# Kernel tuning notes

Measured on AMD Instinct MI355X. Metric: run time of the kernel, lower is better.

The kernel has to match this reference:

```python
import jax, jax.numpy as jnp
import numpy as np

B = 32                 # decode batch (sequences)
NBLK = 128             # blocks per sequence
BLOCK = 16             # tokens per block
H, D = 16, 128         # heads, head_dim
HID = H * D            # 2048
FFN = 8192
VOCAB = 32000
MAXPOS = 8192
KV_LEN = NBLK * BLOCK  # 2048 max context
NUM_BLOCKS = B * NBLK  # 4096
ROPE_THETA = 10000.0


def _rope_cos_sin(pos):
    # pos: [...] int -> cos, sin: [..., D//2]
    inv_freq = 1.0 / (ROPE_THETA ** (jnp.arange(0, D, 2, dtype=jnp.float32) / D))
    ang = pos.astype(jnp.float32)[..., None] * inv_freq
    return jnp.cos(ang), jnp.sin(ang)


def _apply_rope(x, cos, sin):
    # x: [..., D]; cos/sin broadcastable to [..., D//2]; half-split (Llama) rotation
    x1, x2 = jnp.split(x, 2, axis=-1)
    return jnp.concatenate([x1 * cos - x2 * sin, x1 * sin + x2 * cos], axis=-1)


def setup_inputs() -> dict:
    key = jax.random.key(0)
    ks = jax.random.split(key, 12)
    inp = {
        "input_ids": jax.random.randint(ks[0], (B,), 0, VOCAB),
        "positions": jax.random.randint(ks[1], (B,), 0, KV_LEN),
        "kv_cache": jax.random.normal(ks[2], (NUM_BLOCKS, 2, BLOCK, H, D), jnp.float32),
        "block_tables": jnp.arange(NUM_BLOCKS, dtype=jnp.int32).reshape(B, NBLK),
        "context_lens": jax.random.randint(ks[3], (B,), 1, KV_LEN + 1).astype(jnp.int32),
        "embed_tokens": jax.random.normal(ks[4], (VOCAB, HID), jnp.float32) * 0.02,
        "embed_positions": jax.random.normal(ks[5], (MAXPOS, HID), jnp.float32) * 0.02,
        "Wq": jax.random.normal(ks[6], (HID, HID), jnp.float32) / np.float32(np.sqrt(HID)),
        "Wo": jax.random.normal(ks[7], (HID, HID), jnp.float32) / np.float32(np.sqrt(HID)),
        "Wprm": jax.random.normal(ks[8], (HID, HID), jnp.float32) / np.float32(np.sqrt(HID)),
        "W1": jax.random.normal(ks[9], (HID, FFN), jnp.float32) / np.float32(np.sqrt(HID)),
        "W2": jax.random.normal(ks[10], (FFN, HID), jnp.float32) / np.float32(np.sqrt(FFN)),
    }
    return inp


def reference(input_ids, positions, kv_cache, block_tables, context_lens,
              embed_tokens, embed_positions, Wq, Wo, Wprm, W1, W2):
    # token + position embeddings -> [B, HID]
    emb = embed_tokens[input_ids] + embed_positions[positions]

    # query projection with RoPE at the current position (fused RoPE on q)
    q = (emb @ Wq).reshape(B, H, D)
    cos_q, sin_q = _rope_cos_sin(positions)            # [B, D/2]
    q = _apply_rope(q, cos_q[:, None, :], sin_q[:, None, :])

    # paged KV gather: [B, NBLK, 2, BLOCK, H, D]
    kv = kv_cache[block_tables]
    k = kv[:, :, 0].reshape(B, KV_LEN, H, D)
    v = kv[:, :, 1].reshape(B, KV_LEN, H, D)

    # inline RoPE on gathered keys at their cache positions
    tok_pos = jnp.arange(KV_LEN)
    cos_k, sin_k = _rope_cos_sin(tok_pos)              # [S, D/2]
    k = _apply_rope(k, cos_k[None, :, None, :], sin_k[None, :, None, :])

    # decode attention over valid context
    scale = jnp.asarray(D, jnp.float32) ** -0.5
    scores = jnp.einsum("bhd,bshd->bhs", q, k) * scale
    valid = tok_pos[None, :] < context_lens[:, None]   # [B, S]
    scores = jnp.where(valid[:, None, :], scores, jnp.float32(-1e30))
    probs = jax.nn.softmax(scores, axis=-1)
    attn = jnp.einsum("bhs,bshd->bhd", probs, v).reshape(B, HID) @ Wo

    # PRM head + FFN (no activation in source), residual combine
    prm_scores = attn @ Wprm
    ffn_output = (attn @ W1) @ W2
    return ffn_output + prm_scores
```

## Files before the change

### kernel.cpp

```cpp
#include <hip/hip_runtime.h>
#include <hip/hip_bf16.h>
#include <math.h>

#define BATCH   32
#define NBLK    128
#define BLOCK_T 16
#define HEADS   16
#define DHEAD   128
#define HID     2048
#define FFN     8192
#define KV_LEN  2048

#define NSPLIT  16
#define SPLIT_TOKENS 128

__global__ void prep_kernel(const int* __restrict__ ids, const int* __restrict__ pos,
                            const float* __restrict__ et, const float* __restrict__ ep,
                            float* __restrict__ c4f, float* __restrict__ s4f,
                            float* __restrict__ emb) {
    if (blockIdx.x < 512) {
        int s = blockIdx.x * 4 + (threadIdx.x >> 6);
        int i = threadIdx.x & 63;
        float inv = powf(10000.0f, -(float)i / 64.0f);
        float ang = (float)s * inv;
        c4f[s * 64 + i] = cosf(ang);
        s4f[s * 64 + i] = sinf(ang);
    } else {
        int b = blockIdx.x - 512;
        int id = ids[b], p = pos[b];
        const float4* a = (const float4*)(et + (size_t)id * HID);
        const float4* d = (const float4*)(ep + (size_t)p * HID);
        float4* o = (float4*)(emb + (size_t)b * HID);
        for (int c = threadIdx.x; c < HID / 4; c += 256) {
            float4 x = a[c], y = d[c];
            o[c] = make_float4(x.x + y.x, x.y + y.y, x.z + y.z, x.w + y.w);
        }
    }
}

template <int KC>
__device__ __forceinline__ void gemm2_body(
    const float* __restrict__ X, const float* __restrict__ W,
    float* __restrict__ P, int K, int N, int bx, int by, int tid) {
    __shared__ float xs[KC][36];
    const int k0 = by * KC;
    const int j  = bx * 512 + tid * 2;

    #pragma unroll
    for (int t = tid; t < 32 * KC / 4; t += 256) {
        int bb = t / (KC / 4), qq = t % (KC / 4);
        float4 xv = *reinterpret_cast<const float4*>(X + (size_t)bb * K + k0 + 4 * qq);
        xs[4 * qq + 0][bb] = xv.x; xs[4 * qq + 1][bb] = xv.y;
        xs[4 * qq + 2][bb] = xv.z; xs[4 * qq + 3][bb] = xv.w;
    }
    __syncthreads();

    float acc[32][2];
    #pragma unroll
    for (int bb = 0; bb < 32; ++bb) { acc[bb][0] = 0.f; acc[bb][1] = 0.f; }

    const float* wp = W + (size_t)k0 * N + j;
    float2 bufA[16], bufB[16];
    #pragma unroll
    for (int u = 0; u < 16; ++u)
        bufA[u] = *reinterpret_cast<const float2*>(wp + (size_t)u * N);

    #define G2_FMA16(BUF, KK)                                                   \
        _Pragma("unroll")                                                       \
        for (int u = 0; u < 16; ++u) {                                          \
            const float2 w = BUF[u];                                            \
            _Pragma("unroll")                                                   \
            for (int g = 0; g < 8; ++g) {                                       \
                const float4 xv = *reinterpret_cast<const float4*>(&xs[(KK) + u][g * 4]); \
                acc[4*g+0][0] = fmaf(xv.x, w.x, acc[4*g+0][0]);                 \
                acc[4*g+0][1] = fmaf(xv.x, w.y, acc[4*g+0][1]);                 \
                acc[4*g+1][0] = fmaf(xv.y, w.x, acc[4*g+1][0]);                 \
                acc[4*g+1][1] = fmaf(xv.y, w.y, acc[4*g+1][1]);                 \
                acc[4*g+2][0] = fmaf(xv.z, w.x, acc[4*g+2][0]);                 \
                acc[4*g+2][1] = fmaf(xv.z, w.y, acc[4*g+2][1]);                 \
                acc[4*g+3][0] = fmaf(xv.w, w.x, acc[4*g+3][0]);                 \
                acc[4*g+3][1] = fmaf(xv.w, w.y, acc[4*g+3][1]);                 \
            }                                                                   \
        }

    for (int kk = 0; kk < KC; kk += 32) {
        #pragma unroll
        for (int u = 0; u < 16; ++u)
            bufB[u] = *reinterpret_cast<const float2*>(wp + (size_t)(kk + 16 + u) * N);
        G2_FMA16(bufA, kk)
        #pragma unroll
        for (int u = 0; u < 16; ++u) {
            int rr = kk + 32 + u; rr = (rr < KC) ? rr : (KC - 1);
            bufA[u] = *reinterpret_cast<const float2*>(wp + (size_t)rr * N);
        }
        G2_FMA16(bufB, kk + 16)
    }
    #undef G2_FMA16

    float* pp = P + ((size_t)by * 32) * N + j;
    #pragma unroll
    for (int bb = 0; bb < 32; ++bb)
        *reinterpret_cast<float2*>(pp + (size_t)bb * N) = make_float2(acc[bb][0], acc[bb][1]);
}

template <int KC>
__global__ __launch_bounds__(256) void gemm2_kernel(
    const float* __restrict__ X, const float* __restrict__ W,
    float* __restrict__ P, int K, int N) {
    gemm2_body<KC>(X, W, P, K, N, blockIdx.x, blockIdx.y, threadIdx.x);
}

__global__ __launch_bounds__(256) void gemm2_dual_kernel(
    const float* __restrict__ X, const float* __restrict__ Wprm,
    const float* __restrict__ W1,
    float* __restrict__ Pprm, float* __restrict__ P1) {
    if (blockIdx.x < 256) {
        gemm2_body<32>(X, Wprm, Pprm, HID, HID, blockIdx.x & 3, blockIdx.x >> 2, threadIdx.x);
    } else {
        int bb = blockIdx.x - 256;
        gemm2_body<128>(X, W1, P1, HID, FFN, bb & 15, bb >> 4, threadIdx.x);
    }
}

__global__ void red_stage1(const float* __restrict__ PA, const float* __restrict__ PB,
                           int ngA, float* __restrict__ S, int total4) {
    int idx4 = blockIdx.x * 256 + threadIdx.x;
    if (idx4 >= total4) return;
    int g = blockIdx.y;
    const float4* src = (const float4*)((g < ngA) ? PA : PB);
    int c0 = ((g < ngA) ? g : (g - ngA)) * 8;
    float4 s = make_float4(0.f, 0.f, 0.f, 0.f);
    #pragma unroll
    for (int c = 0; c < 8; ++c) {
        float4 v = src[(size_t)(c0 + c) * total4 + idx4];
        s.x += v.x; s.y += v.y; s.z += v.z; s.w += v.w;
    }
    ((float4*)S)[(size_t)g * total4 + idx4] = s;
}

__global__ void red_stage2(const float* __restrict__ S, int ng, int total4,
                           float* __restrict__ out) {
    int idx4 = blockIdx.x * 256 + threadIdx.x;
    if (idx4 >= total4) return;
    float4 s = make_float4(0.f, 0.f, 0.f, 0.f);
    for (int g = 0; g < ng; ++g) {
        float4 v = ((const float4*)S)[(size_t)g * total4 + idx4];
        s.x += v.x; s.y += v.y; s.z += v.z; s.w += v.w;
    }
    ((float4*)out)[idx4] = s;
}

__global__ void reduce4_kernel(const float* __restrict__ P, int nch, int total4,
                               float* __restrict__ out) {
    int idx4 = blockIdx.x * 256 + threadIdx.x;
    if (idx4 >= total4) return;
    const float4* P4 = (const float4*)P;
    float4 s = make_float4(0.f, 0.f, 0.f, 0.f);
    for (int c = 0; c < nch; ++c) {
        float4 v = P4[(size_t)c * total4 + idx4];
        s.x += v.x; s.y += v.y; s.z += v.z; s.w += v.w;
    }
    ((float4*)out)[idx4] = s;
}

__global__ void rope_q_from_S(const float* __restrict__ S, int ng,
                              const int* __restrict__ positions,
                              const float* __restrict__ c4f, const float* __restrict__ s4f,
                              float* __restrict__ qout) {
    int idx = blockIdx.x * 256 + threadIdx.x;
    int i = idx & 63, hh = (idx >> 6) & 15, b = idx >> 10;
    int base = b * HID + hh * DHEAD;
    float q1 = 0.f, q2 = 0.f;
    for (int g = 0; g < ng; ++g) {
        q1 += S[(size_t)g * (BATCH * HID) + base + i];
        q2 += S[(size_t)g * (BATCH * HID) + base + 64 + i];
    }
    int pos = positions[b];
    float co = c4f[pos * 64 + i], si = s4f[pos * 64 + i];
    qout[base + i]      = q1 * co - q2 * si;
    qout[base + 64 + i] = q1 * si + q2 * co;
}

__global__ __launch_bounds__(256) void attn_partial_kernel(
    const float* __restrict__ q, const float* __restrict__ kv,
    const int* __restrict__ block_tables, const int* __restrict__ context_lens,
    const float* __restrict__ c4f, const float* __restrict__ s4f,
    float* __restrict__ pm, float* __restrict__ pl, float* __restrict__ pacc) {
    const int idx = blockIdx.x;
    const int split = idx & (NSPLIT - 1);
    const int h = (idx >> 4) & 15;
    const int b = idx >> 8;
    const int wave = threadIdx.x >> 6, lane = threadIdx.x & 63, l5 = lane & 31;
    const int r = wave * 2 + (lane >> 5);

    const int ctx = context_lens[b];
    const int s_begin = split * SPLIT_TOKENS;
    const int len = min(SPLIT_TOKENS, ctx - s_begin);

    __shared__ int bt[8];
    __shared__ float sm8[8], sl8[8];
    __shared__ float4 sacc[8][32];
    if (threadIdx.x < 8)
        bt[threadIdx.x] = block_tables[b * NBLK + split * 8 + threadIdx.x];
    __syncthreads();

    const float4 q4 = *reinterpret_cast<const float4*>(q + b * HID + h * DHEAD + 4 * l5);
    const float sgn = (l5 & 16) ? 1.f : -1.f;
    const int fq4 = (l5 & 15) * 4;

    float m = -INFINITY, l = 0.f;
    float4 a4 = make_float4(0.f, 0.f, 0.f, 0.f);

    if (len > 0) {
        const int nt = (len + 7) >> 3;
        const int NI = (nt + 3) & ~3;

        #define LOADT(T, K4, V4, C4, S4) {                                         \
            int tc = min((T), len - 1);                                            \
            const float* kp = kv + (size_t)bt[tc >> 4] * 65536                     \
                                 + (size_t)(tc & 15) * 2048 + h * DHEAD;           \
            K4 = *reinterpret_cast<const float4*>(kp + 4 * l5);                    \
            V4 = *reinterpret_cast<const float4*>(kp + 32768 + 4 * l5);            \
            C4 = *reinterpret_cast<const float4*>(c4f + (size_t)(s_begin + tc) * 64 + fq4); \
            float4 stmp = *reinterpret_cast<const float4*>(s4f + (size_t)(s_begin + tc) * 64 + fq4); \
            S4 = make_float4(stmp.x * sgn, stmp.y * sgn, stmp.z * sgn, stmp.w * sgn); \
        }

        #define PROCT(T, K4, V4, C4, S4) {                                         \
            float4 pk;                                                             \
            pk.x = __shfl_xor(K4.x, 16); pk.y = __shfl_xor(K4.y, 16);              \
            pk.z = __shfl_xor(K4.z, 16); pk.w = __shfl_xor(K4.w, 16);              \
            float krx = fmaf(pk.x, S4.x, K4.x * C4.x);                             \
            float kry = fmaf(pk.y, S4.y, K4.y * C4.y);                             \
            float krz = fmaf(pk.z, S4.z, K4.z * C4.z);                             \
            float krw = fmaf(pk.w, S4.w, K4.w * C4.w);                             \
            float dot = q4.x * krx + q4.y * kry + q4.z * krz + q4.w * krw;         \
            dot += __shfl_xor(dot, 1);  dot += __shfl_xor(dot, 2);                 \
            dot += __shfl_xor(dot, 4);  dot += __shfl_xor(dot, 8);                 \
            dot += __shfl_xor(dot, 16);                                            \
            float d = ((T) < len) ? dot * 0.08838834764831845f : -INFINITY;        \
            float mn = fmaxf(m, d);                                                \
            float ms = fmaxf(mn, -3.0e38f);                                        \
            float corr = __expf(m - ms);                                           \
            float e = __expf(d - ms);                                              \
            l = l * corr + e;                                                      \
            a4.x = fmaf(e, V4.x, a4.x * corr);                                     \
            a4.y = fmaf(e, V4.y, a4.y * corr);                                     \
            a4.z = fmaf(e, V4.z, a4.z * corr);                                     \
            a4.w = fmaf(e, V4.w, a4.w * corr);                                     \
            m = mn;                                                                \
        }

        float4 kA, vA, cA, sA, kB, vB, cB, sB;
        float4 kC, vC, cC, sC, kD, vD, cD, sD;
        LOADT(r,      kA, vA, cA, sA);
        LOADT(r + 8,  kB, vB, cB, sB);
        LOADT(r + 16, kC, vC, cC, sC);
        LOADT(r + 24, kD, vD, cD, sD);

        for (int i = 0; i < NI; i += 4) {
            int t = r + 8 * i;
            PROCT(t,      kA, vA, cA, sA);  LOADT(t + 32, kA, vA, cA, sA);
            PROCT(t + 8,  kB, vB, cB, sB);  LOADT(t + 40, kB, vB, cB, sB);
            PROCT(t + 16, kC, vC, cC, sC);  LOADT(t + 48, kC, vC, cC, sC);
            PROCT(t + 24, kD, vD, cD, sD);  LOADT(t + 56, kD, vD, cD, sD);
        }
        #undef LOADT
        #undef PROCT
    }

    if (l5 == 0) { sm8[r] = m; sl8[r] = l; }
    sacc[r][l5] = a4;
    __syncthreads();

    if (threadIdx.x < 32) {
        float M = -INFINITY;
        #pragma unroll
        for (int rr = 0; rr < 8; ++rr) M = fmaxf(M, sm8[rr]);
        float L = 0.f;
        float4 o = make_float4(0.f, 0.f, 0.f, 0.f);
        #pragma unroll
        for (int rr = 0; rr < 8; ++rr) {
            float ew = (sm8[rr] == -INFINITY) ? 0.f : __expf(sm8[rr] - M);
            L += sl8[rr] * ew;
            float4 v = sacc[rr][threadIdx.x];
            o.x = fmaf(v.x, ew, o.x); o.y = fmaf(v.y, ew, o.y);
            o.z = fmaf(v.z, ew, o.z); o.w = fmaf(v.w, ew, o.w);
        }
        if (threadIdx.x == 0) { pm[idx] = M; pl[idx] = L; }
        *reinterpret_cast<float4*>(pacc + (size_t)idx * 128 + 4 * threadIdx.x) = o;
    }
}

__global__ void attn_combine_kernel(const float* __restrict__ pm, const float* __restrict__ pl,
                                    const float* __restrict__ pacc, float* __restrict__ attn_out) {
    const int bh = blockIdx.x;
    const int l5 = threadIdx.x;
    if (l5 >= 32) return;
    const int base = bh * NSPLIT;
    float M = -INFINITY;
    #pragma unroll
    for (int sp = 0; sp < NSPLIT; ++sp) M = fmaxf(M, pm[base + sp]);
    float L = 0.f;
    float4 o = make_float4(0.f, 0.f, 0.f, 0.f);
    #pragma unroll
    for (int sp = 0; sp < NSPLIT; ++sp) {
        float mv = pm[base + sp];
        float ew = (mv == -INFINITY) ? 0.f : __expf(mv - M);
        L += pl[base + sp] * ew;
        float4 v = *reinterpret_cast<const float4*>(pacc + (size_t)(base + sp) * 128 + 4 * l5);
        o.x = fmaf(v.x, ew, o.x); o.y = fmaf(v.y, ew, o.y);
        o.z = fmaf(v.z, ew, o.z); o.w = fmaf(v.w, ew, o.w);
    }
    float inv = 1.f / L;
    *reinterpret_cast<float4*>(attn_out + bh * 128 + 4 * l5) =
        make_float4(o.x * inv, o.y * inv, o.z * inv, o.w * inv);
}

extern "C" void kernel_launch(void* const* d_in, const int* in_sizes, int n_in,
                              void* d_out, int out_size, void* d_ws, size_t ws_size,
                              hipStream_t stream) {
    const int*   input_ids    = (const int*)d_in[0];
    const int*   positions    = (const int*)d_in[1];
    const float* kv_cache     = (const float*)d_in[2];
    const int*   block_tables = (const int*)d_in[3];
    const int*   context_lens = (const int*)d_in[4];
    const float* embed_tokens = (const float*)d_in[5];
    const float* embed_pos    = (const float*)d_in[6];
    const float* Wq  = (const float*)d_in[7];
    const float* Wo  = (const float*)d_in[8];
    const float* Wprm= (const float*)d_in[9];
    const float* W1  = (const float*)d_in[10];
    const float* W2  = (const float*)d_in[11];
    float* out = (float*)d_out;

    char* ws = (char*)d_ws;
    size_t off = 0;
    float* c4f  = (float*)(ws + off); off += (size_t)KV_LEN * 64 * 4;
    float* s4f  = (float*)(ws + off); off += (size_t)KV_LEN * 64 * 4;
    float* emb  = (float*)(ws + off); off += (size_t)BATCH * HID * 4;
    float* qbuf = (float*)(ws + off); off += (size_t)BATCH * HID * 4;
    float* attn = (float*)(ws + off); off += (size_t)BATCH * HID * 4;
    float* ao   = (float*)(ws + off); off += (size_t)BATCH * HID * 4;
    float* h1   = (float*)(ws + off); off += (size_t)BATCH * FFN * 4;
    float* pm   = (float*)(ws + off); off += (size_t)BATCH * HEADS * NSPLIT * 4;
    float* plv  = (float*)(ws + off); off += (size_t)BATCH * HEADS * NSPLIT * 4;
    float* pacc = (float*)(ws + off); off += (size_t)BATCH * HEADS * NSPLIT * 128 * 4;
    float* S    = (float*)(ws + off); off += (size_t)16 * BATCH * HID * 4;
    float* P    = (float*)(ws + off); off += (size_t)64 * BATCH * FFN * 4;
    float* Pprm = (float*)(ws + off); off += (size_t)64 * BATCH * HID * 4;
    (void)ws_size; (void)in_sizes; (void)n_in; (void)out_size;

    const int T4_HID = BATCH * HID / 4;
    const int T4_FFN = BATCH * FFN / 4;

    prep_kernel<<<544, 256, 0, stream>>>(input_ids, positions, embed_tokens, embed_pos,
                                         c4f, s4f, emb);
    gemm2_kernel<32><<<dim3(4, 64), 256, 0, stream>>>(emb, Wq, P, HID, HID);
    red_stage1<<<dim3(64, 8), 256, 0, stream>>>(P, P, 8, S, T4_HID);
    rope_q_from_S<<<128, 256, 0, stream>>>(S, 8, positions, c4f, s4f, qbuf);
    attn_partial_kernel<<<BATCH * HEADS * NSPLIT, 256, 0, stream>>>(
        qbuf, kv_cache, block_tables, context_lens, c4f, s4f, pm, plv, pacc);
    attn_combine_kernel<<<BATCH * HEADS, 64, 0, stream>>>(pm, plv, pacc, attn);
    gemm2_kernel<32><<<dim3(4, 64), 256, 0, stream>>>(attn, Wo, P, HID, HID);
    red_stage1<<<dim3(64, 8), 256, 0, stream>>>(P, P, 8, S, T4_HID);
    red_stage2<<<64, 256, 0, stream>>>(S, 8, T4_HID, ao);
    gemm2_dual_kernel<<<512, 256, 0, stream>>>(ao, Wprm, W1, Pprm, P);
    reduce4_kernel<<<256, 256, 0, stream>>>(P, 16, T4_FFN, h1);
    gemm2_kernel<128><<<dim3(4, 64), 256, 0, stream>>>(h1, W2, P, FFN, HID);
    red_stage1<<<dim3(64, 16), 256, 0, stream>>>(P, Pprm, 8, S, T4_HID);
    red_stage2<<<64, 256, 0, stream>>>(S, 16, T4_HID, out);
}
```

Baseline: 294.9 us.

## Fuse partial-sum reductions into GEMM loaders and q RoPE into attention

Removes the standalone reduce and RoPE-q kernels: GEMM X-tile loaders now sum the split-K partial buffers on the fly (NRED template), and attention reads the 8 partial q slices, reduces them and applies RoPE in-register. The attention inner loop is restructured to apply RoPE to q per token instead of to K (algebraic transfer), and processes 4 tokens per online-softmax update with separate K and V prefetch. This cuts kernel launches and intermediate round trips through global memory, but each GEMM block now redundantly reads partial buffers (up to 16x for W2 input) and each attention block re-reads 8 q partials.

Result: slower. 348.2 us (+18.1%).

```diff
diff --git a/kernel.cpp b/kernel.cpp
--- a/kernel.cpp
+++ b/kernel.cpp
@@ -38,7 +38,7 @@
     }
 }
 
-template <int KC>
+template <int KC, int NRED>
 __device__ __forceinline__ void gemm2_body(
     const float* __restrict__ X, const float* __restrict__ W,
     float* __restrict__ P, int K, int N, int bx, int by, int tid) {
@@ -49,7 +49,13 @@
     #pragma unroll
     for (int t = tid; t < 32 * KC / 4; t += 256) {
         int bb = t / (KC / 4), qq = t % (KC / 4);
-        float4 xv = *reinterpret_cast<const float4*>(X + (size_t)bb * K + k0 + 4 * qq);
+        const float* xp = X + (size_t)bb * K + k0 + 4 * qq;
+        float4 xv = make_float4(0.f, 0.f, 0.f, 0.f);
+        #pragma unroll
+        for (int c = 0; c < NRED; ++c) {
+            float4 v = *reinterpret_cast<const float4*>(xp + (size_t)c * 32 * K);
+            xv.x += v.x; xv.y += v.y; xv.z += v.z; xv.w += v.w;
+        }
         xs[4 * qq + 0][bb] = xv.x; xs[4 * qq + 1][bb] = xv.y;
         xs[4 * qq + 2][bb] = xv.z; xs[4 * qq + 3][bb] = xv.w;
     }
@@ -103,22 +109,22 @@
         *reinterpret_cast<float2*>(pp + (size_t)bb * N) = make_float2(acc[bb][0], acc[bb][1]);
 }
 
-template <int KC>
+template <int KC, int NRED>
 __global__ __launch_bounds__(256) void gemm2_kernel(
     const float* __restrict__ X, const float* __restrict__ W,
     float* __restrict__ P, int K, int N) {
-    gemm2_body<KC>(X, W, P, K, N, blockIdx.x, blockIdx.y, threadIdx.x);
+    gemm2_body<KC, NRED>(X, W, P, K, N, blockIdx.x, blockIdx.y, threadIdx.x);
 }
 
 __global__ __launch_bounds__(256) void gemm2_dual_kernel(
-    const float* __restrict__ X, const float* __restrict__ Wprm,
+    const float* __restrict__ S, const float* __restrict__ Wprm,
     const float* __restrict__ W1,
     float* __restrict__ Pprm, float* __restrict__ P1) {
     if (blockIdx.x < 256) {
-        gemm2_body<32>(X, Wprm, Pprm, HID, HID, blockIdx.x & 3, blockIdx.x >> 2, threadIdx.x);
+        gemm2_body<32, 8>(S, Wprm, Pprm, HID, HID, blockIdx.x & 3, blockIdx.x >> 2, threadIdx.x);
     } else {
         int bb = blockIdx.x - 256;
-        gemm2_body<128>(X, W1, P1, HID, FFN, bb & 15, bb >> 4, threadIdx.x);
+        gemm2_body<128, 8>(S, W1, P1, HID, FFN, bb & 15, bb >> 4, threadIdx.x);
     }
 }
 
@@ -150,39 +156,9 @@
     ((float4*)out)[idx4] = s;
 }
 
-__global__ void reduce4_kernel(const float* __restrict__ P, int nch, int total4,
-                               float* __restrict__ out) {
-    int idx4 = blockIdx.x * 256 + threadIdx.x;
-    if (idx4 >= total4) return;
-    const float4* P4 = (const float4*)P;
-    float4 s = make_float4(0.f, 0.f, 0.f, 0.f);
-    for (int c = 0; c < nch; ++c) {
-        float4 v = P4[(size_t)c * total4 + idx4];
-        s.x += v.x; s.y += v.y; s.z += v.z; s.w += v.w;
-    }
-    ((float4*)out)[idx4] = s;
-}
-
-__global__ void rope_q_from_S(const float* __restrict__ S, int ng,
-                              const int* __restrict__ positions,
-                              const float* __restrict__ c4f, const float* __restrict__ s4f,
-                              float* __restrict__ qout) {
-    int idx = blockIdx.x * 256 + threadIdx.x;
-    int i = idx & 63, hh = (idx >> 6) & 15, b = idx >> 10;
-    int base = b * HID + hh * DHEAD;
-    float q1 = 0.f, q2 = 0.f;
-    for (int g = 0; g < ng; ++g) {
-        q1 += S[(size_t)g * (BATCH * HID) + base + i];
-        q2 += S[(size_t)g * (BATCH * HID) + base + 64 + i];
-    }
-    int pos = positions[b];
-    float co = c4f[pos * 64 + i], si = s4f[pos * 64 + i];
-    qout[base + i]      = q1 * co - q2 * si;
-    qout[base + 64 + i] = q1 * si + q2 * co;
-}
-
 __global__ __launch_bounds__(256) void attn_partial_kernel(
-    const float* __restrict__ q, const float* __restrict__ kv,
+    const float* __restrict__ S, const int* __restrict__ positions,
+    const float* __restrict__ kv,
     const int* __restrict__ block_tables, const int* __restrict__ context_lens,
     const float* __restrict__ c4f, const float* __restrict__ s4f,
     float* __restrict__ pm, float* __restrict__ pl, float* __restrict__ pacc) {
@@ -202,71 +178,106 @@
     __shared__ float4 sacc[8][32];
     if (threadIdx.x < 8)
         bt[threadIdx.x] = block_tables[b * NBLK + split * 8 + threadIdx.x];
+
+    const int fq4 = (l5 & 15) * 4;
+    const int pos = positions[b];
+    float4 qa = make_float4(0.f, 0.f, 0.f, 0.f);
+    {
+        const float* Sq = S + (size_t)b * HID + h * DHEAD + 4 * l5;
+        #pragma unroll
+        for (int g = 0; g < 8; ++g) {
+            float4 v = *reinterpret_cast<const float4*>(Sq + (size_t)g * (BATCH * HID));
+            qa.x += v.x; qa.y += v.y; qa.z += v.z; qa.w += v.w;
+        }
+    }
+    const float sgnQ = (l5 & 16) ? 1.f : -1.f;
+    float4 cq = *reinterpret_cast<const float4*>(c4f + pos * 64 + fq4);
+    float4 sq = *reinterpret_cast<const float4*>(s4f + pos * 64 + fq4);
+    float4 qp;
+    qp.x = __shfl_xor(qa.x, 16); qp.y = __shfl_xor(qa.y, 16);
+    qp.z = __shfl_xor(qa.z, 16); qp.w = __shfl_xor(qa.w, 16);
+    float4 qr;
+    qr.x = fmaf(sgnQ * qp.x, sq.x, qa.x * cq.x);
+    qr.y = fmaf(sgnQ * qp.y, sq.y, qa.y * cq.y);
+    qr.z = fmaf(sgnQ * qp.z, sq.z, qa.z * cq.z);
+    qr.w = fmaf(sgnQ * qp.w, sq.w, qa.w * cq.w);
+    float4 pqs;
+    pqs.x = -sgnQ * __shfl_xor(qr.x, 16); pqs.y = -sgnQ * __shfl_xor(qr.y, 16);
+    pqs.z = -sgnQ * __shfl_xor(qr.z, 16); pqs.w = -sgnQ * __shfl_xor(qr.w, 16);
     __syncthreads();
-
-    const float4 q4 = *reinterpret_cast<const float4*>(q + b * HID + h * DHEAD + 4 * l5);
-    const float sgn = (l5 & 16) ? 1.f : -1.f;
-    const int fq4 = (l5 & 15) * 4;
 
     float m = -INFINITY, l = 0.f;
     float4 a4 = make_float4(0.f, 0.f, 0.f, 0.f);
 
     if (len > 0) {
         const int nt = (len + 7) >> 3;
-        const int NI = (nt + 3) & ~3;
-
-        #define LOADT(T, K4, V4, C4, S4) {                                         \
-            int tc = min((T), len - 1);                                            \
+        const int NI = (nt + 7) & ~7;
+
+        #define LKCS(SEQ, K4, C4, S4) {                                            \
+            int tc = min(r + 8 * (SEQ), len - 1);                                  \
             const float* kp = kv + (size_t)bt[tc >> 4] * 65536                     \
                                  + (size_t)(tc & 15) * 2048 + h * DHEAD;           \
             K4 = *reinterpret_cast<const float4*>(kp + 4 * l5);                    \
+            C4 = *reinterpret_cast<const float4*>(c4f + (size_t)(s_begin + tc) * 64 + fq4); \
+            S4 = *reinterpret_cast<const float4*>(s4f + (size_t)(s_begin + tc) * 64 + fq4); \
+        }
+        #define LV(SEQ, V4) {                                                      \
+            int tc = min(r + 8 * (SEQ), len - 1);                                  \
+            const float* kp = kv + (size_t)bt[tc >> 4] * 65536                     \
+                                 + (size_t)(tc & 15) * 2048 + h * DHEAD;           \
             V4 = *reinterpret_cast<const float4*>(kp + 32768 + 4 * l5);            \
-            C4 = *reinterpret_cast<const float4*>(c4f + (size_t)(s_begin + tc) * 64 + fq4); \
-            float4 stmp = *reinterpret_cast<const float4*>(s4f + (size_t)(s_begin + tc) * 64 + fq4); \
-            S4 = make_float4(stmp.x * sgn, stmp.y * sgn, stmp.z * sgn, stmp.w * sgn); \
-        }
-
-        #define PROCT(T, K4, V4, C4, S4) {                                         \
-            float4 pk;                                                             \
-            pk.x = __shfl_xor(K4.x, 16); pk.y = __shfl_xor(K4.y, 16);              \
-            pk.z = __shfl_xor(K4.z, 16); pk.w = __shfl_xor(K4.w, 16);              \
-            float krx = fmaf(pk.x, S4.x, K4.x * C4.x);                             \
-            float kry = fmaf(pk.y, S4.y, K4.y * C4.y);                             \
-            float krz = fmaf(pk.z, S4.z, K4.z * C4.z);                             \
-            float krw = fmaf(pk.w, S4.w, K4.w * C4.w);                             \
-            float dot = q4.x * krx + q4.y * kry + q4.z * krz + q4.w * krw;         \
-            dot += __shfl_xor(dot, 1);  dot += __shfl_xor(dot, 2);                 \
-            dot += __shfl_xor(dot, 4);  dot += __shfl_xor(dot, 8);                 \
-            dot += __shfl_xor(dot, 16);                                            \
-            float d = ((T) < len) ? dot * 0.08838834764831845f : -INFINITY;        \
-            float mn = fmaxf(m, d);                                                \
+        }
+        #define DOTT(SEQ, K4, C4, S4, DOUT) {                                      \
+            float cfx = fmaf(pqs.x, S4.x, qr.x * C4.x);                            \
+            float cfy = fmaf(pqs.y, S4.y, qr.y * C4.y);                            \
+            float cfz = fmaf(pqs.z, S4.z, qr.z * C4.z);                            \
+            float cfw = fmaf(pqs.w, S4.w, qr.w * C4.w);                            \
+            float dd = fmaf(K4.x, cfx, fmaf(K4.y, cfy, fmaf(K4.z, cfz, K4.w * cfw))); \
+            dd += __shfl_xor(dd, 1);  dd += __shfl_xor(dd, 2);                     \
+            dd += __shfl_xor(dd, 4);  dd += __shfl_xor(dd, 8);                     \
+            dd += __shfl_xor(dd, 16);                                              \
+            DOUT = (r + 8 * (SEQ) < len) ? dd * 0.08838834764831845f : -INFINITY;  \
+        }
+        #define UPD(D0, D1, D2, D3, V0, V1, V2, V3) {                              \
+            float gm = fmaxf(fmaxf(D0, D1), fmaxf(D2, D3));                        \
+            float mn = fmaxf(m, gm);                                               \
             float ms = fmaxf(mn, -3.0e38f);                                        \
             float corr = __expf(m - ms);                                           \
-            float e = __expf(d - ms);                                              \
-            l = l * corr + e;                                                      \
-            a4.x = fmaf(e, V4.x, a4.x * corr);                                     \
-            a4.y = fmaf(e, V4.y, a4.y * corr);                                     \
-            a4.z = fmaf(e, V4.z, a4.z * corr);                                     \
-            a4.w = fmaf(e, V4.w, a4.w * corr);                                     \
+            float e0 = __expf(D0 - ms), e1 = __expf(D1 - ms);                      \
+            float e2 = __expf(D2 - ms), e3 = __expf(D3 - ms);                      \
+            l = fmaf(l, corr, e0 + e1 + e2 + e3);                                  \
+            a4.x = fmaf(e3, V3.x, fmaf(e2, V2.x, fmaf(e1, V1.x, fmaf(e0, V0.x, a4.x * corr)))); \
+            a4.y = fmaf(e3, V3.y, fmaf(e2, V2.y, fmaf(e1, V1.y, fmaf(e0, V0.y, a4.y * corr)))); \
+            a4.z = fmaf(e3, V3.z, fmaf(e2, V2.z, fmaf(e1, V1.z, fmaf(e0, V0.z, a4.z * corr)))); \
+            a4.w = fmaf(e3, V3.w, fmaf(e2, V2.w, fmaf(e1, V1.w, fmaf(e0, V0.w, a4.w * corr)))); \
             m = mn;                                                                \
         }
 
-        float4 kA, vA, cA, sA, kB, vB, cB, sB;
-        float4 kC, vC, cC, sC, kD, vD, cD, sD;
-        LOADT(r,      kA, vA, cA, sA);
-        LOADT(r + 8,  kB, vB, cB, sB);
-        LOADT(r + 16, kC, vC, cC, sC);
-        LOADT(r + 24, kD, vD, cD, sD);
-
-        for (int i = 0; i < NI; i += 4) {
-            int t = r + 8 * i;
-            PROCT(t,      kA, vA, cA, sA);  LOADT(t + 32, kA, vA, cA, sA);
-            PROCT(t + 8,  kB, vB, cB, sB);  LOADT(t + 40, kB, vB, cB, sB);
-            PROCT(t + 16, kC, vC, cC, sC);  LOADT(t + 48, kC, vC, cC, sC);
-            PROCT(t + 24, kD, vD, cD, sD);  LOADT(t + 56, kD, vD, cD, sD);
-        }
-        #undef LOADT
-        #undef PROCT
+        float4 kA, cA, sA, kB, cB, sB, kC, cC, sC, kD, cD, sD;
+        float4 vA0, vA1, vA2, vA3, vB0, vB1, vB2, vB3;
+        LKCS(0, kA, cA, sA); LKCS(1, kB, cB, sB);
+        LKCS(2, kC, cC, sC); LKCS(3, kD, cD, sD);
+        LV(0, vA0); LV(1, vA1); LV(2, vA2); LV(3, vA3);
+
+        for (int n = 0; n < NI; n += 8) {
+            float d0, d1, d2, d3;
+            DOTT(n + 0, kA, cA, sA, d0);  LKCS(n + 4, kA, cA, sA);
+            DOTT(n + 1, kB, cB, sB, d1);  LKCS(n + 5, kB, cB, sB);
+            DOTT(n + 2, kC, cC, sC, d2);  LKCS(n + 6, kC, cC, sC);
+            DOTT(n + 3, kD, cD, sD, d3);  LKCS(n + 7, kD, cD, sD);
+            LV(n + 4, vB0); LV(n + 5, vB1); LV(n + 6, vB2); LV(n + 7, vB3);
+            UPD(d0, d1, d2, d3, vA0, vA1, vA2, vA3);
+            DOTT(n + 4, kA, cA, sA, d0);  LKCS(n + 8,  kA, cA, sA);
+            DOTT(n + 5, kB, cB, sB, d1);  LKCS(n + 9,  kB, cB, sB);
+            DOTT(n + 6, kC, cC, sC, d2);  LKCS(n + 10, kC, cC, sC);
+            DOTT(n + 7, kD, cD, sD, d3);  LKCS(n + 11, kD, cD, sD);
+            LV(n + 8, vA0); LV(n + 9, vA1); LV(n + 10, vA2); LV(n + 11, vA3);
+            UPD(d0, d1, d2, d3, vB0, vB1, vB2, vB3);
+        }
+        #undef LKCS
+        #undef LV
+        #undef DOTT
+        #undef UPD
     }
 
     if (l5 == 0) { sm8[r] = m; sl8[r] = l; }
@@ -339,35 +350,29 @@
     float* c4f  = (float*)(ws + off); off += (size_t)KV_LEN * 64 * 4;
     float* s4f  = (float*)(ws + off); off += (size_t)KV_LEN * 64 * 4;
     float* emb  = (float*)(ws + off); off += (size_t)BATCH * HID * 4;
-    float* qbuf = (float*)(ws + off); off += (size_t)BATCH * HID * 4;
     float* attn = (float*)(ws + off); off += (size_t)BATCH * HID * 4;
-    float* ao   = (float*)(ws + off); off += (size_t)BATCH * HID * 4;
-    float* h1   = (float*)(ws + off); off += (size_t)BATCH * FFN * 4;
     float* pm   = (float*)(ws + off); off += (size_t)BATCH * HEADS * NSPLIT * 4;
     float* plv  = (float*)(ws + off); off += (size_t)BATCH * HEADS * NSPLIT * 4;
     float* pacc = (float*)(ws + off); off += (size_t)BATCH * HEADS * NSPLIT * 128 * 4;
     float* S    = (float*)(ws + off); off += (size_t)16 * BATCH * HID * 4;
-    float* P    = (float*)(ws + off); off += (size_t)64 * BATCH * FFN * 4;
+    float* P    = (float*)(ws + off); off += (size_t)64 * BATCH * HID * 4;
+    float* P1   = (float*)(ws + off); off += (size_t)16 * BATCH * FFN * 4;
     float* Pprm = (float*)(ws + off); off += (size_t)64 * BATCH * HID * 4;
     (void)ws_size; (void)in_sizes; (void)n_in; (void)out_size;
 
     const int T4_HID = BATCH * HID / 4;
-    const int T4_FFN = BATCH * FFN / 4;
 
     prep_kernel<<<544, 256, 0, stream>>>(input_ids, positions, embed_tokens, embed_pos,
                                          c4f, s4f, emb);
-    gemm2_kernel<32><<<dim3(4, 64), 256, 0, stream>>>(emb, Wq, P, HID, HID);
+    gemm2_kernel<32, 1><<<dim3(4, 64), 256, 0, stream>>>(emb, Wq, P, HID, HID);
     red_stage1<<<dim3(64, 8), 256, 0, stream>>>(P, P, 8, S, T4_HID);
-    rope_q_from_S<<<128, 256, 0, stream>>>(S, 8, positions, c4f, s4f, qbuf);
     attn_partial_kernel<<<BATCH * HEADS * NSPLIT, 256, 0, stream>>>(
-        qbuf, kv_cache, block_tables, context_lens, c4f, s4f, pm, plv, pacc);
+        S, positions, kv_cache, block_tables, context_lens, c4f, s4f, pm, plv, pacc);
     attn_combine_kernel<<<BATCH * HEADS, 64, 0, stream>>>(pm, plv, pacc, attn);
-    gemm2_kernel<32><<<dim3(4, 64), 256, 0, stream>>>(attn, Wo, P, HID, HID);
+    gemm2_kernel<32, 1><<<dim3(4, 64), 256, 0, stream>>>(attn, Wo, P, HID, HID);
     red_stage1<<<dim3(64, 8), 256, 0, stream>>>(P, P, 8, S, T4_HID);
-    red_stage2<<<64, 256, 0, stream>>>(S, 8, T4_HID, ao);
-    gemm2_dual_kernel<<<512, 256, 0, stream>>>(ao, Wprm, W1, Pprm, P);
-    reduce4_kernel<<<256, 256, 0, stream>>>(P, 16, T4_FFN, h1);
-    gemm2_kernel<128><<<dim3(4, 64), 256, 0, stream>>>(h1, W2, P, FFN, HID);
+    gemm2_dual_kernel<<<512, 256, 0, stream>>>(S, Wprm, W1, Pprm, P1);
+    gemm2_kernel<128, 16><<<dim3(4, 64), 256, 0, stream>>>(P1, W2, P, FFN, HID);
     red_stage1<<<dim3(64, 16), 256, 0, stream>>>(P, Pprm, 8, S, T4_HID);
     red_stage2<<<64, 256, 0, stream>>>(S, 16, T4_HID, out);
 }
```
